# Kernel tuning notes

Hardware: AMD Instinct MI355X
Metric: run time of the kernel (lower is better)

Reference implementation:

```python
import jax, jax.numpy as jnp
import numpy as np

N = 4096
IN_DIM = 256
HID = 64
NHEADS = 4
OUT_DIM = 128
ALPHA = 0.5  # LeakyReLU negative slope
NEG_INF = -9e15


def gat_layer(x, mask, W, a, concat):
    """Dense GraphAttentionLayer (pyGAT style).
    x:[N,Fin], mask:[N,N] bool, W:[Fin,Fout], a:[2*Fout]."""
    Wh = x @ W                                   # [N, Fout]
    Fout = W.shape[1]
    f1 = Wh @ a[:Fout]                           # [N]
    f2 = Wh @ a[Fout:]                           # [N]
    e = jax.nn.leaky_relu(f1[:, None] + f2[None, :], negative_slope=ALPHA)  # [N,N]
    att = jax.nn.softmax(jnp.where(mask, e, NEG_INF), axis=1)               # [N,N]
    h = att @ Wh                                 # [N, Fout]
    return jax.nn.elu(h) if concat else h


def setup_inputs() -> dict:
    key = jax.random.key(0)
    ks = jax.random.split(key, 6)
    x = jax.random.normal(ks[0], (N, IN_DIM), dtype=jnp.float32)
    adj = jax.random.randint(ks[1], (N, N), 0, 2, dtype=jnp.int32)
    s_in = 1.0 / np.sqrt(IN_DIM)
    s_hid = 1.0 / np.sqrt(HID * NHEADS)
    W_heads = jax.random.uniform(ks[2], (NHEADS, IN_DIM, HID), jnp.float32, -s_in, s_in)
    a_heads = jax.random.uniform(ks[3], (NHEADS, 2 * HID), jnp.float32, -s_in, s_in)
    W_out = jax.random.uniform(ks[4], (HID * NHEADS, OUT_DIM), jnp.float32, -s_hid, s_hid)
    a_out = jax.random.uniform(ks[5], (2 * OUT_DIM,), jnp.float32, -s_hid, s_hid)
    return {"x": x, "adj": adj, "W_heads": W_heads, "a_heads": a_heads,
            "W_out": W_out, "a_out": a_out}


def reference(x, adj, W_heads, a_heads, W_out, a_out):
    mask = adj > 0
    # multi-head attention, concat along feature dim
    heads = jax.vmap(lambda W, a: gat_layer(x, mask, W, a, True))(W_heads, a_heads)
    h = jnp.transpose(heads, (1, 0, 2)).reshape(N, NHEADS * HID)  # [N, H*HID]
    # dropout=0 -> identity; final GAT layer (concat=False) + outer ELU
    out = jax.nn.elu(gat_layer(h, mask, W_out, a_out, False))     # [N, OUT_DIM]
    return out
```

## Files before the change

### kernel.cpp

```cpp
#include <hip/hip_runtime.h>
#include <hip/hip_bf16.h>

#define N 4096
#define IN_DIM 256
#define HID 64
#define NHEADS 4
#define OUT_DIM 128
#define LOG2E 1.44269504088896340736f

typedef __attribute__((ext_vector_type(8))) short bf16x8;
typedef __attribute__((ext_vector_type(4))) float f32x4;

__device__ __forceinline__ ushort2 bsplit(float v) {
    const ushort h = __hip_bfloat16_raw(__float2bfloat16(v)).x;
    const float vh = __uint_as_float((unsigned)h << 16);
    const ushort l = __hip_bfloat16_raw(__float2bfloat16(v - vh)).x;
    return make_ushort2(h, l);
}

__global__ __launch_bounds__(256, 4) void prep_kernel(
        const float* __restrict__ x, const float* __restrict__ W,
        const float* __restrict__ a, const int* __restrict__ adj,
        __hip_bfloat16* __restrict__ WhB,
        float* __restrict__ C1, float* __restrict__ E2, float* __restrict__ S2,
        unsigned* __restrict__ maskT) {
    const int t = threadIdx.x;
    if (blockIdx.x < 256) {
        const int h = t >> 6, lane = t & 63, m = lane & 15, quad = lane >> 4;
        const int i0 = blockIdx.x * 16;
        const float* xrow = x + (size_t)(i0 + m) * IN_DIM;
        const float* Wp = W + (size_t)h * IN_DIM * HID;
        const f32x4 zero = {0.f, 0.f, 0.f, 0.f};
        f32x4 acc[4] = {zero, zero, zero, zero};
        for (int ks = 0; ks < 8; ks++) {
            const int kb = ks * 32 + quad * 8;
            const float4 xa = *(const float4*)(xrow + kb);
            const float4 xb = *(const float4*)(xrow + kb + 4);
            const float xf[8] = {xa.x, xa.y, xa.z, xa.w, xb.x, xb.y, xb.z, xb.w};
            bf16x8 xh, xl;
#pragma unroll
            for (int e = 0; e < 8; e++) {
                const ushort2 s = bsplit(xf[e]);
                xh[e] = (short)s.x; xl[e] = (short)s.y;
            }
#pragma unroll
            for (int ct = 0; ct < 4; ct++) {
                bf16x8 wh, wl;
#pragma unroll
                for (int e = 0; e < 8; e++) {
                    const ushort2 s =
                        bsplit(Wp[(size_t)(kb + e) * HID + ct * 16 + m]);
                    wh[e] = (short)s.x; wl[e] = (short)s.y;
                }
                acc[ct] = __builtin_amdgcn_mfma_f32_16x16x32_bf16(
                    xh, wh, acc[ct], 0, 0, 0);
                acc[ct] = __builtin_amdgcn_mfma_f32_16x16x32_bf16(
                    xl, wh, acc[ct], 0, 0, 0);
                acc[ct] = __builtin_amdgcn_mfma_f32_16x16x32_bf16(
                    xh, wl, acc[ct], 0, 0, 0);
            }
        }
        const int jblk = i0 >> 5, jb2 = (i0 >> 4) & 1;
#pragma unroll
        for (int ct = 0; ct < 4; ct++) {
#pragma unroll
            for (int r = 0; r < 4; r++) {
                const int jo = quad * 4 + r;
                const int lane_idx = m + 16 * (2 * jb2 + (jo >> 3));
                WhB[((((size_t)h * (N / 32) + jblk) * 4 + ct) * 64 + lane_idx) *
                        8 + (jo & 7)] = __float2bfloat16(acc[ct][r]);
            }
        }
        float av1[4], av2[4];
#pragma unroll
        for (int ct = 0; ct < 4; ct++) {
            av1[ct] = a[h * 2 * HID + ct * 16 + m];
            av2[ct] = a[h * 2 * HID + HID + ct * 16 + m];
        }
        float s1[4], s2[4];
#pragma unroll
        for (int r = 0; r < 4; r++) {
            s1[r] = 0.f; s2[r] = 0.f;
#pragma unroll
            for (int ct = 0; ct < 4; ct++) {
                s1[r] += acc[ct][r] * av1[ct];
                s2[r] += acc[ct][r] * av2[ct];
            }
        }
#pragma unroll
        for (int mm = 8; mm > 0; mm >>= 1) {
#pragma unroll
            for (int r = 0; r < 4; r++) {
                s1[r] += __shfl_xor(s1[r], mm, 64);
                s2[r] += __shfl_xor(s2[r], mm, 64);
            }
        }
        if (m == 0) {
#pragma unroll
            for (int r = 0; r < 4; r++) {
                const size_t ix = (size_t)h * N + i0 + quad * 4 + r;
                C1[ix] = __builtin_amdgcn_exp2f(s1[r] * (-0.5f * LOG2E));
                E2[ix] = __builtin_amdgcn_exp2f(s2[r] * LOG2E);
                S2[ix] = __builtin_amdgcn_exp2f(s2[r] * (0.5f * LOG2E));
            }
        }
    } else {
        const int lane = t & 63, w = t >> 6;
        const int i = (blockIdx.x - 256) * 4 + w;
        const int4* arow = (const int4*)(adj + (size_t)i * N);
        for (int jb = 0; jb < N / 256; jb++) {
            const int4 a4 = arow[jb * 64 + lane];
            unsigned long long bal[4];
            bal[0] = __ballot(a4.x > 0);
            bal[1] = __ballot(a4.y > 0);
            bal[2] = __ballot(a4.z > 0);
            bal[3] = __ballot(a4.w > 0);
            if (lane < 8) {
                unsigned word = 0;
#pragma unroll
                for (int e = 0; e < 4; e++) {
                    unsigned xv = (unsigned)(bal[e] >> (8 * lane)) & 0xFFu;
                    xv = (xv | (xv << 12)) & 0x000F000Fu;
                    xv = (xv | (xv << 6))  & 0x03030303u;
                    xv = (xv | (xv << 3))  & 0x11111111u;
                    word |= xv << e;
                }
                maskT[(size_t)(jb * 8 + lane) * N + i] = word;
            }
        }
    }
}

template <int HEADS, int D, int DSL, int G, int MW, int OCC>
__global__ __launch_bounds__(G * 64, OCC) void attn_fused(
        const unsigned* __restrict__ maskT,
        const __hip_bfloat16* __restrict__ WhB,
        const float* __restrict__ C1g, const float* __restrict__ E2g,
        const float* __restrict__ S2g,
        float* __restrict__ outp) {
    constexpr int CTtot = D / 16;
    constexpr int CTT = CTtot / DSL;
    constexpr int CC = (D == 64) ? 1 : 2;
    constexpr int KSTEPS = N / (32 * G);
    static_assert(KSTEPS % 2 == 0, "two-step pipeline needs even KSTEPS");
    __shared__ float sh[MW * G * 16 * CC * 17];
    __shared__ float dsh[MW * G * 16];
    const int t = threadIdx.x;
    const int g = t >> 6, lane = t & 63;
    const int m = lane & 15, quad = lane >> 4;
    const int h = blockIdx.y / DSL, slc = blockIdx.y % DSL;
    const int i0 = blockIdx.x * (16 * MW);

    float c1v[MW];
#pragma unroll
    for (int mw = 0; mw < MW; mw++)
        c1v[mw] = C1g[(size_t)h * N + i0 + mw * 16 + m];

    const unsigned* mp = maskT + (size_t)(g * KSTEPS) * N + i0 + m;
    const float* ep = E2g + (size_t)h * N + g * (N / G) + quad * 8;
    const float* sp = S2g + (size_t)h * N + g * (N / G) + quad * 8;
    const bf16x8* bp = (const bf16x8*)WhB +
                       ((size_t)h * (N / 32) * CTtot +
                        (size_t)(g * KSTEPS) * CTtot + slc * CTT) * 64 + lane;

    const f32x4 zero = {0.f, 0.f, 0.f, 0.f};
    f32x4 acc[MW][CTT];
    f32x4 sac[MW];
#pragma unroll
    for (int mw = 0; mw < MW; mw++) {
        sac[mw] = zero;
#pragma unroll
        for (int ct = 0; ct < CTT; ct++) acc[mw][ct] = zero;
    }
    const short one_bf = (short)0x3F80;
    const bf16x8 ones = {one_bf, one_bf, one_bf, one_bf,
                         one_bf, one_bf, one_bf, one_bf};

    unsigned mwrdA[MW], mwrdB[MW];
    float4 e2loA, e2hiA, s2loA, s2hiA;
    float4 e2loB, e2hiB, s2loB, s2hiB;
    bf16x8 bfragA[CTT], bfragB[CTT];

    auto stage = [&](auto& mwrd_, float4& e2lo_, float4& e2hi_,
                     float4& s2lo_, float4& s2hi_, auto& bfrag_) {
#pragma unroll
        for (int mw = 0; mw < MW; mw++) mwrd_[mw] = mp[mw * 16];
        e2lo_ = *(const float4*)(ep);
        e2hi_ = *(const float4*)(ep + 4);
        s2lo_ = *(const float4*)(sp);
        s2hi_ = *(const float4*)(sp + 4);
#pragma unroll
        for (int ct = 0; ct < CTT; ct++) bfrag_[ct] = bp[ct * 64];
        mp += N; ep += 32; sp += 32; bp += CTtot * 64;
    };

    auto compute = [&](const auto& mwrd_, const float4& e2lo_,
                       const float4& e2hi_, const float4& s2lo_,
                       const float4& s2hi_, const auto& bfrag_) {
        const float Ee[8] = {e2lo_.x, e2lo_.y, e2lo_.z, e2lo_.w,
                             e2hi_.x, e2hi_.y, e2hi_.z, e2hi_.w};
        const float Se[8] = {s2lo_.x, s2lo_.y, s2lo_.z, s2lo_.w,
                             s2hi_.x, s2hi_.y, s2hi_.z, s2hi_.w};
        bf16x8 afr[MW];
#pragma unroll
        for (int mw = 0; mw < MW; mw++) {
            const unsigned mword = (mwrd_[mw] >> (quad * 8)) & 0xFFu;
            const unsigned spread = mword * 0x8001u;
            float p[8];
#pragma unroll
            for (int e = 0; e < 8; e++)
                p[e] = fmaxf(Ee[e], c1v[mw] * Se[e]);
            union { bf16x8 v; unsigned u32[4]; __hip_bfloat162 h2[4]; } u;
#pragma unroll
            for (int e2 = 0; e2 < 4; e2++) {
                u.h2[e2] = __float22bfloat162_rn(
                    make_float2(p[2 * e2], p[2 * e2 + 1]));
                const unsigned mk =
                    ((spread >> (2 * e2)) & 0x00010001u) * 0xFFFFu;
                u.u32[e2] &= mk;
            }
            afr[mw] = u.v;
        }
#pragma unroll
        for (int ct = 0; ct < CTT; ct++)
#pragma unroll
            for (int mw = 0; mw < MW; mw++)
                acc[mw][ct] = __builtin_amdgcn_mfma_f32_16x16x32_bf16(
                    afr[mw], bfrag_[ct], acc[mw][ct], 0, 0, 0);
#pragma unroll
        for (int mw = 0; mw < MW; mw++)
            sac[mw] = __builtin_amdgcn_mfma_f32_16x16x32_bf16(
                afr[mw], ones, sac[mw], 0, 0, 0);
    };

    stage(mwrdA, e2loA, e2hiA, s2loA, s2hiA, bfragA);
    for (int ks = 0; ks < KSTEPS; ks += 2) {
        stage(mwrdB, e2loB, e2hiB, s2loB, s2hiB, bfragB);
        compute(mwrdA, e2loA, e2hiA, s2loA, s2hiA, bfragA);
        if (ks + 2 < KSTEPS)
            stage(mwrdA, e2loA, e2hiA, s2loA, s2hiA, bfragA);
        compute(mwrdB, e2loB, e2hiB, s2loB, s2hiB, bfragB);
    }

#pragma unroll
    for (int rd = 0; rd < CTT / CC; rd++) {
#pragma unroll
        for (int mw = 0; mw < MW; mw++) {
#pragma unroll
            for (int cc = 0; cc < CC; cc++) {
#pragma unroll
                for (int r = 0; r < 4; r++)
                    sh[(((mw * G + g) * 16 + quad * 4 + r) * CC + cc) * 17 + m] =
                        acc[mw][rd * CC + cc][r];
            }
            if (rd == 0 && m == 0) {
#pragma unroll
                for (int r = 0; r < 4; r++)
                    dsh[(mw * G + g) * 16 + quad * 4 + r] = sac[mw][r];
            }
        }
        __syncthreads();
        if (t < 16 * CC * 16) {
            int row, chl;
            if (D == 64) { row = t & 15; chl = (t >> 4) & 15; }
            else         { chl = t & 31; row = (t >> 5) & 15; }
#pragma unroll
            for (int mw = 0; mw < MW; mw++) {
                float av = 0.f, ss = 0.f;
#pragma unroll
                for (int gg = 0; gg < G; gg++) {
                    av += sh[(((mw * G + gg) * 16 + row) * CC + (chl >> 4)) * 17 +
                             (chl & 15)];
                    ss += dsh[(mw * G + gg) * 16 + row];
                }
                float v = av / ss;
                v = (v > 0.f) ? v : (__builtin_amdgcn_exp2f(v * LOG2E) - 1.f);
                const int chg = h * D + slc * (CTT * 16) + rd * CC * 16 + chl;
                const int irow = i0 + mw * 16 + row;
                if (D == 64)
                    outp[(size_t)irow * (NHEADS * HID) + chg] = v;
                else
                    outp[(size_t)irow * D + chg] = v;
            }
        }
        __syncthreads();
    }
}

__global__ __launch_bounds__(512, 2) void gemm2_kernel(
        const float* __restrict__ h1, const float* __restrict__ W2,
        const float* __restrict__ a2, __hip_bfloat16* __restrict__ WhB2,
        float* __restrict__ C1, float* __restrict__ E2, float* __restrict__ S2) {
    __shared__ float fred[8][16][2];
    const int t = threadIdx.x;
    const int w = t >> 6, lane = t & 63, m = lane & 15, quad = lane >> 4;
    const int i0 = blockIdx.x * 16;
    const float* arow = h1 + (size_t)(i0 + m) * IN_DIM;
    const float* wp = W2 + w * 16 + m;
    const f32x4 zero = {0.f, 0.f, 0.f, 0.f};
    f32x4 acc = zero;
    for (int ks = 0; ks < 8; ks++) {
        const int kb = ks * 32 + quad * 8;
        const float4 xa = *(const float4*)(arow + kb);
        const float4 xb = *(const float4*)(arow + kb + 4);
        const float xf[8] = {xa.x, xa.y, xa.z, xa.w, xb.x, xb.y, xb.z, xb.w};
        bf16x8 xh, xl, wh, wl;
#pragma unroll
        for (int e = 0; e < 8; e++) {
            const ushort2 s = bsplit(xf[e]);
            xh[e] = (short)s.x; xl[e] = (short)s.y;
        }
#pragma unroll
        for (int e = 0; e < 8; e++) {
            const ushort2 s = bsplit(wp[(size_t)(kb + e) * OUT_DIM]);
            wh[e] = (short)s.x; wl[e] = (short)s.y;
        }
        acc = __builtin_amdgcn_mfma_f32_16x16x32_bf16(xh, wh, acc, 0, 0, 0);
        acc = __builtin_amdgcn_mfma_f32_16x16x32_bf16(xl, wh, acc, 0, 0, 0);
        acc = __builtin_amdgcn_mfma_f32_16x16x32_bf16(xh, wl, acc, 0, 0, 0);
    }
    const int jblk = i0 >> 5, jb2 = (i0 >> 4) & 1;
#pragma unroll
    for (int r = 0; r < 4; r++) {
        const int jo = quad * 4 + r;
        const int lane_idx = m + 16 * (2 * jb2 + (jo >> 3));
        WhB2[(((size_t)jblk * 8 + w) * 64 + lane_idx) * 8 + (jo & 7)] =
            __float2bfloat16(acc[r]);
    }
    const float av1 = a2[w * 16 + m], av2 = a2[OUT_DIM + w * 16 + m];
    float s1[4], s2[4];
#pragma unroll
    for (int r = 0; r < 4; r++) { s1[r] = acc[r] * av1; s2[r] = acc[r] * av2; }
#pragma unroll
    for (int mm = 8; mm > 0; mm >>= 1) {
#pragma unroll
        for (int r = 0; r < 4; r++) {
            s1[r] += __shfl_xor(s1[r], mm, 64);
            s2[r] += __shfl_xor(s2[r], mm, 64);
        }
    }
    if (m == 0) {
#pragma unroll
        for (int r = 0; r < 4; r++) {
            fred[w][quad * 4 + r][0] = s1[r];
            fred[w][quad * 4 + r][1] = s2[r];
        }
    }
    __syncthreads();
    if (t < 32) {
        const int row = t & 15, fn = t >> 4;
        float s = 0.f;
#pragma unroll
        for (int w8 = 0; w8 < 8; w8++) s += fred[w8][row][fn];
        if (fn) {
            E2[i0 + row] = __builtin_amdgcn_exp2f(s * LOG2E);
            S2[i0 + row] = __builtin_amdgcn_exp2f(s * (0.5f * LOG2E));
        } else {
            C1[i0 + row] = __builtin_amdgcn_exp2f(s * (-0.5f * LOG2E));
        }
    }
}

extern "C" void kernel_launch(void* const* d_in, const int* in_sizes, int n_in,
                              void* d_out, int out_size, void* d_ws, size_t ws_size,
                              hipStream_t stream) {
    const float* x   = (const float*)d_in[0];
    const int*   adj = (const int*)d_in[1];
    const float* Wh_ = (const float*)d_in[2];
    const float* ah  = (const float*)d_in[3];
    const float* W2  = (const float*)d_in[4];
    const float* a2  = (const float*)d_in[5];
    float* out = (float*)d_out;

    float* ws = (float*)d_ws;
    float* C1a = ws;
    float* E2a = C1a + (size_t)NHEADS * N;
    float* S2a = E2a + (size_t)NHEADS * N;
    float* C1b = S2a + (size_t)NHEADS * N;
    float* E2b = C1b + N;
    float* S2b = E2b + N;
    float* h1  = S2b + N;
    __hip_bfloat16* WhB1 = (__hip_bfloat16*)(h1 + (size_t)IN_DIM * N);
    __hip_bfloat16* WhB2 = WhB1 + (size_t)NHEADS * HID * N;
    unsigned* maskT = (unsigned*)(WhB2 + (size_t)OUT_DIM * N);

    prep_kernel<<<1280, 256, 0, stream>>>(x, Wh_, ah, adj, WhB1,
                                          C1a, E2a, S2a, maskT);
    attn_fused<NHEADS, HID, 1, 8, 2, 2>
        <<<dim3(N / 32, NHEADS), 512, 0, stream>>>(maskT, WhB1,
                                                   C1a, E2a, S2a, h1);
    gemm2_kernel<<<N / 16, 512, 0, stream>>>(h1, W2, a2, WhB2,
                                             C1b, E2b, S2b);
    attn_fused<1, OUT_DIM, 1, 8, 1, 2>
        <<<dim3(N / 16, 1), 512, 0, stream>>>(maskT, WhB2,
                                              C1b, E2b, S2b, out);
}
```

Measured before the change: 166.9 us.

## Fuse layer-1 multi-head attention with second-layer projection GEMM

Replaces the layer-1 attention kernel and the separate gemm2 kernel with one kernel. Each block handles 16 rows across all four heads, keeps the concatenated hidden features in shared memory, and computes W_out projection plus attention logits in place. This removes the h1 round trip through global memory and one kernel launch. In exchange the grid shrinks from 512 blocks of 32 rows to 256 blocks of 16 rows, the mask is read once per block instead of once per head, and register and shared-memory pressure rises.

```diff
diff --git a/kernel.cpp b/kernel.cpp
--- a/kernel.cpp
+++ b/kernel.cpp
@@ -131,6 +131,199 @@
     }
 }
 
+__global__ __launch_bounds__(512, 2) void attn1_gemm2(
+        const unsigned* __restrict__ maskT,
+        const __hip_bfloat16* __restrict__ WhB1,
+        const float* __restrict__ C1a, const float* __restrict__ E2a,
+        const float* __restrict__ S2a,
+        const float* __restrict__ W2, const float* __restrict__ a2,
+        __hip_bfloat16* __restrict__ WhB2,
+        float* __restrict__ C1b, float* __restrict__ E2b,
+        float* __restrict__ S2b) {
+    constexpr int G = 8;
+    constexpr int KSTEPS = N / (32 * G);
+    __shared__ float sh[8704];
+    __shared__ float dsh[128];
+    __shared__ float h1s[16 * 260];
+    __shared__ float fred[8 * 16 * 2];
+    const int t = threadIdx.x;
+    const int g = t >> 6, lane = t & 63;
+    const int m = lane & 15, quad = lane >> 4;
+    const int i0 = blockIdx.x * 16;
+
+    const float c1v0 = C1a[0 * N + i0 + m];
+    const float c1v1 = C1a[1 * N + i0 + m];
+    const float c1v2 = C1a[2 * N + i0 + m];
+    const float c1v3 = C1a[3 * N + i0 + m];
+
+    const unsigned* mp = maskT + (size_t)(g * KSTEPS) * N + i0 + m;
+    const int tb = g * (N / G) + quad * 8;
+    const float* ep0 = E2a + 0 * N + tb; const float* sp0 = S2a + 0 * N + tb;
+    const float* ep1 = E2a + 1 * N + tb; const float* sp1 = S2a + 1 * N + tb;
+    const float* ep2 = E2a + 2 * N + tb; const float* sp2 = S2a + 2 * N + tb;
+    const float* ep3 = E2a + 3 * N + tb; const float* sp3 = S2a + 3 * N + tb;
+    const bf16x8* bbase = (const bf16x8*)WhB1 + (size_t)(g * KSTEPS) * 4 * 64 + lane;
+    const bf16x8* bp0 = bbase + (size_t)0 * (N / 32) * 4 * 64;
+    const bf16x8* bp1 = bbase + (size_t)1 * (N / 32) * 4 * 64;
+    const bf16x8* bp2 = bbase + (size_t)2 * (N / 32) * 4 * 64;
+    const bf16x8* bp3 = bbase + (size_t)3 * (N / 32) * 4 * 64;
+
+    const f32x4 zero = {0.f, 0.f, 0.f, 0.f};
+    f32x4 acc0[4] = {zero, zero, zero, zero};
+    f32x4 acc1[4] = {zero, zero, zero, zero};
+    f32x4 acc2[4] = {zero, zero, zero, zero};
+    f32x4 acc3[4] = {zero, zero, zero, zero};
+    f32x4 sac0 = zero, sac1 = zero, sac2 = zero, sac3 = zero;
+    const short one_bf = (short)0x3F80;
+    const bf16x8 ones = {one_bf, one_bf, one_bf, one_bf,
+                         one_bf, one_bf, one_bf, one_bf};
+
+    for (int ks = 0; ks < KSTEPS; ks++) {
+        const unsigned mwrd = *mp; mp += N;
+        const unsigned mword = (mwrd >> (quad * 8)) & 0xFFu;
+        const unsigned spread = mword * 0x8001u;
+
+        auto headstep = [&](float c1, const float*& ep_, const float*& sp_,
+                            const bf16x8*& bp_, f32x4 (&acc_)[4], f32x4& sac_) {
+            const float4 e2lo = *(const float4*)(ep_);
+            const float4 e2hi = *(const float4*)(ep_ + 4);
+            const float4 s2lo = *(const float4*)(sp_);
+            const float4 s2hi = *(const float4*)(sp_ + 4);
+            ep_ += 32; sp_ += 32;
+            bf16x8 bf0 = bp_[0 * 64], bf1 = bp_[1 * 64];
+            bf16x8 bf2 = bp_[2 * 64], bf3 = bp_[3 * 64];
+            bp_ += 4 * 64;
+            const float Ee[8] = {e2lo.x, e2lo.y, e2lo.z, e2lo.w,
+                                 e2hi.x, e2hi.y, e2hi.z, e2hi.w};
+            const float Se[8] = {s2lo.x, s2lo.y, s2lo.z, s2lo.w,
+                                 s2hi.x, s2hi.y, s2hi.z, s2hi.w};
+            float p[8];
+#pragma unroll
+            for (int e = 0; e < 8; e++)
+                p[e] = fmaxf(Ee[e], c1 * Se[e]);
+            union { bf16x8 v; unsigned u32[4]; __hip_bfloat162 h2[4]; } u;
+#pragma unroll
+            for (int e2 = 0; e2 < 4; e2++) {
+                u.h2[e2] = __float22bfloat162_rn(
+                    make_float2(p[2 * e2], p[2 * e2 + 1]));
+                const unsigned mk =
+                    ((spread >> (2 * e2)) & 0x00010001u) * 0xFFFFu;
+                u.u32[e2] &= mk;
+            }
+            const bf16x8 afr = u.v;
+            acc_[0] = __builtin_amdgcn_mfma_f32_16x16x32_bf16(afr, bf0, acc_[0], 0, 0, 0);
+            acc_[1] = __builtin_amdgcn_mfma_f32_16x16x32_bf16(afr, bf1, acc_[1], 0, 0, 0);
+            acc_[2] = __builtin_amdgcn_mfma_f32_16x16x32_bf16(afr, bf2, acc_[2], 0, 0, 0);
+            acc_[3] = __builtin_amdgcn_mfma_f32_16x16x32_bf16(afr, bf3, acc_[3], 0, 0, 0);
+            sac_ = __builtin_amdgcn_mfma_f32_16x16x32_bf16(afr, ones, sac_, 0, 0, 0);
+        };
+        headstep(c1v0, ep0, sp0, bp0, acc0, sac0);
+        headstep(c1v1, ep1, sp1, bp1, acc1, sac1);
+        headstep(c1v2, ep2, sp2, bp2, acc2, sac2);
+        headstep(c1v3, ep3, sp3, bp3, acc3, sac3);
+    }
+
+    auto epi = [&](f32x4 (&acc_)[4], f32x4& sac_, int hh) {
+#pragma unroll
+        for (int ct = 0; ct < 4; ct++)
+#pragma unroll
+            for (int r = 0; r < 4; r++)
+                sh[(g * 16 + quad * 4 + r) * 68 + ct * 17 + m] = acc_[ct][r];
+        if (m == 0) {
+#pragma unroll
+            for (int r = 0; r < 4; r++)
+                dsh[g * 16 + quad * 4 + r] = sac_[r];
+        }
+        __syncthreads();
+        if (t < 256) {
+            const int row = t >> 4, col = t & 15;
+            float ss = 0.f;
+#pragma unroll
+            for (int gg = 0; gg < G; gg++) ss += dsh[gg * 16 + row];
+#pragma unroll
+            for (int ct = 0; ct < 4; ct++) {
+                float av = 0.f;
+#pragma unroll
+                for (int gg = 0; gg < G; gg++)
+                    av += sh[(gg * 16 + row) * 68 + ct * 17 + col];
+                float v = av / ss;
+                v = (v > 0.f) ? v : (__builtin_amdgcn_exp2f(v * LOG2E) - 1.f);
+                h1s[row * 260 + hh * 64 + ct * 16 + col] = v;
+            }
+        }
+        __syncthreads();
+    };
+    epi(acc0, sac0, 0);
+    epi(acc1, sac1, 1);
+    epi(acc2, sac2, 2);
+    epi(acc3, sac3, 3);
+
+    {
+        const float* wp = W2 + g * 16 + m;
+        f32x4 gacc = zero;
+        for (int ks2 = 0; ks2 < 8; ks2++) {
+            const int kb = ks2 * 32 + quad * 8;
+            float xf[8];
+#pragma unroll
+            for (int e = 0; e < 8; e++) xf[e] = h1s[m * 260 + kb + e];
+            bf16x8 xh, xl, wh, wl;
+#pragma unroll
+            for (int e = 0; e < 8; e++) {
+                const ushort2 s = bsplit(xf[e]);
+                xh[e] = (short)s.x; xl[e] = (short)s.y;
+            }
+#pragma unroll
+            for (int e = 0; e < 8; e++) {
+                const ushort2 s = bsplit(wp[(size_t)(kb + e) * OUT_DIM]);
+                wh[e] = (short)s.x; wl[e] = (short)s.y;
+            }
+            gacc = __builtin_amdgcn_mfma_f32_16x16x32_bf16(xh, wh, gacc, 0, 0, 0);
+            gacc = __builtin_amdgcn_mfma_f32_16x16x32_bf16(xl, wh, gacc, 0, 0, 0);
+            gacc = __builtin_amdgcn_mfma_f32_16x16x32_bf16(xh, wl, gacc, 0, 0, 0);
+        }
+        const int jblk = i0 >> 5, jb2 = (i0 >> 4) & 1;
+#pragma unroll
+        for (int r = 0; r < 4; r++) {
+            const int jo = quad * 4 + r;
+            const int lane_idx = m + 16 * (2 * jb2 + (jo >> 3));
+            WhB2[(((size_t)jblk * 8 + g) * 64 + lane_idx) * 8 + (jo & 7)] =
+                __float2bfloat16(gacc[r]);
+        }
+        const float av1 = a2[g * 16 + m], av2 = a2[OUT_DIM + g * 16 + m];
+        float s1[4], s2[4];
+#pragma unroll
+        for (int r = 0; r < 4; r++) { s1[r] = gacc[r] * av1; s2[r] = gacc[r] * av2; }
+#pragma unroll
+        for (int mm = 8; mm > 0; mm >>= 1) {
+#pragma unroll
+            for (int r = 0; r < 4; r++) {
+                s1[r] += __shfl_xor(s1[r], mm, 64);
+                s2[r] += __shfl_xor(s2[r], mm, 64);
+            }
+        }
+        if (m == 0) {
+#pragma unroll
+            for (int r = 0; r < 4; r++) {
+                fred[(g * 16 + quad * 4 + r) * 2 + 0] = s1[r];
+                fred[(g * 16 + quad * 4 + r) * 2 + 1] = s2[r];
+            }
+        }
+        __syncthreads();
+        if (t < 32) {
+            const int row = t & 15, fn = t >> 4;
+            float s = 0.f;
+#pragma unroll
+            for (int w8 = 0; w8 < 8; w8++) s += fred[(w8 * 16 + row) * 2 + fn];
+            if (fn) {
+                E2b[i0 + row] = __builtin_amdgcn_exp2f(s * LOG2E);
+                S2b[i0 + row] = __builtin_amdgcn_exp2f(s * (0.5f * LOG2E));
+            } else {
+                C1b[i0 + row] = __builtin_amdgcn_exp2f(s * (-0.5f * LOG2E));
+            }
+        }
+    }
+}
+
 template <int HEADS, int D, int DSL, int G, int MW, int OCC>
 __global__ __launch_bounds__(G * 64, OCC) void attn_fused(
         const unsigned* __restrict__ maskT,
@@ -287,80 +480,6 @@
     }
 }
 
-__global__ __launch_bounds__(512, 2) void gemm2_kernel(
-        const float* __restrict__ h1, const float* __restrict__ W2,
-        const float* __restrict__ a2, __hip_bfloat16* __restrict__ WhB2,
-        float* __restrict__ C1, float* __restrict__ E2, float* __restrict__ S2) {
-    __shared__ float fred[8][16][2];
-    const int t = threadIdx.x;
-    const int w = t >> 6, lane = t & 63, m = lane & 15, quad = lane >> 4;
-    const int i0 = blockIdx.x * 16;
-    const float* arow = h1 + (size_t)(i0 + m) * IN_DIM;
-    const float* wp = W2 + w * 16 + m;
-    const f32x4 zero = {0.f, 0.f, 0.f, 0.f};
-    f32x4 acc = zero;
-    for (int ks = 0; ks < 8; ks++) {
-        const int kb = ks * 32 + quad * 8;
-        const float4 xa = *(const float4*)(arow + kb);
-        const float4 xb = *(const float4*)(arow + kb + 4);
-        const float xf[8] = {xa.x, xa.y, xa.z, xa.w, xb.x, xb.y, xb.z, xb.w};
-        bf16x8 xh, xl, wh, wl;
-#pragma unroll
-        for (int e = 0; e < 8; e++) {
-            const ushort2 s = bsplit(xf[e]);
-            xh[e] = (short)s.x; xl[e] = (short)s.y;
-        }
-#pragma unroll
-        for (int e = 0; e < 8; e++) {
-            const ushort2 s = bsplit(wp[(size_t)(kb + e) * OUT_DIM]);
-            wh[e] = (short)s.x; wl[e] = (short)s.y;
-        }
-        acc = __builtin_amdgcn_mfma_f32_16x16x32_bf16(xh, wh, acc, 0, 0, 0);
-        acc = __builtin_amdgcn_mfma_f32_16x16x32_bf16(xl, wh, acc, 0, 0, 0);
-        acc = __builtin_amdgcn_mfma_f32_16x16x32_bf16(xh, wl, acc, 0, 0, 0);
-    }
-    const int jblk = i0 >> 5, jb2 = (i0 >> 4) & 1;
-#pragma unroll
-    for (int r = 0; r < 4; r++) {
-        const int jo = quad * 4 + r;
-        const int lane_idx = m + 16 * (2 * jb2 + (jo >> 3));
-        WhB2[(((size_t)jblk * 8 + w) * 64 + lane_idx) * 8 + (jo & 7)] =
-            __float2bfloat16(acc[r]);
-    }
-    const float av1 = a2[w * 16 + m], av2 = a2[OUT_DIM + w * 16 + m];
-    float s1[4], s2[4];
-#pragma unroll
-    for (int r = 0; r < 4; r++) { s1[r] = acc[r] * av1; s2[r] = acc[r] * av2; }
-#pragma unroll
-    for (int mm = 8; mm > 0; mm >>= 1) {
-#pragma unroll
-        for (int r = 0; r < 4; r++) {
-            s1[r] += __shfl_xor(s1[r], mm, 64);
-            s2[r] += __shfl_xor(s2[r], mm, 64);
-        }
-    }
-    if (m == 0) {
-#pragma unroll
-        for (int r = 0; r < 4; r++) {
-            fred[w][quad * 4 + r][0] = s1[r];
-            fred[w][quad * 4 + r][1] = s2[r];
-        }
-    }
-    __syncthreads();
-    if (t < 32) {
-        const int row = t & 15, fn = t >> 4;
-        float s = 0.f;
-#pragma unroll
-        for (int w8 = 0; w8 < 8; w8++) s += fred[w8][row][fn];
-        if (fn) {
-            E2[i0 + row] = __builtin_amdgcn_exp2f(s * LOG2E);
-            S2[i0 + row] = __builtin_amdgcn_exp2f(s * (0.5f * LOG2E));
-        } else {
-            C1[i0 + row] = __builtin_amdgcn_exp2f(s * (-0.5f * LOG2E));
-        }
-    }
-}
-
 extern "C" void kernel_launch(void* const* d_in, const int* in_sizes, int n_in,
                               void* d_out, int out_size, void* d_ws, size_t ws_size,
                               hipStream_t stream) {
@@ -386,11 +505,8 @@
 
     prep_kernel<<<1280, 256, 0, stream>>>(x, Wh_, ah, adj, WhB1,
                                           C1a, E2a, S2a, maskT);
-    attn_fused<NHEADS, HID, 1, 8, 2, 2>
-        <<<dim3(N / 32, NHEADS), 512, 0, stream>>>(maskT, WhB1,
-                                                   C1a, E2a, S2a, h1);
-    gemm2_kernel<<<N / 16, 512, 0, stream>>>(h1, W2, a2, WhB2,
-                                             C1b, E2b, S2b);
+    attn1_gemm2<<<N / 16, 512, 0, stream>>>(maskT, WhB1, C1a, E2a, S2a,
+                                            W2, a2, WhB2, C1b, E2b, S2b);
     attn_fused<1, OUT_DIM, 1, 8, 1, 2>
         <<<dim3(N / 16, 1), 512, 0, stream>>>(maskT, WhB2,
                                               C1b, E2b, S2b, out);
```

Result: slower. 240.1 us (+43.8%).
